# Kernel tuning notes

Hardware: AMD Instinct MI355X
Metric: run time of the kernel (lower is better)

## Reference

```python
import jax, jax.numpy as jnp
import numpy as np

D_MODEL = 1024
HEADS = 16
D_K = D_MODEL // HEADS
D_FF = 4096
EPS = 1e-6


def setup_inputs() -> dict:
    key = jax.random.key(0)
    ks = jax.random.split(key, 20)
    B, S, D = 8, 1024, D_MODEL
    sc = 1.0 / np.sqrt(D)
    scf = 1.0 / np.sqrt(D_FF)
    inp = {
        "x": jax.random.normal(ks[0], (B, S, D), jnp.float32),
        "mask": jnp.ones((B, 1, 1, S), jnp.int32),
        "wq": jax.random.normal(ks[1], (D, D), jnp.float32) * sc,
        "bq": jnp.zeros((D,), jnp.float32),
        "wk": jax.random.normal(ks[2], (D, D), jnp.float32) * sc,
        "bk": jnp.zeros((D,), jnp.float32),
        "wv": jax.random.normal(ks[3], (D, D), jnp.float32) * sc,
        "bv": jnp.zeros((D,), jnp.float32),
        "wo": jax.random.normal(ks[4], (D, D), jnp.float32) * sc,
        "bo": jnp.zeros((D,), jnp.float32),
        "w1": jax.random.normal(ks[5], (D_FF, D), jnp.float32) * sc,
        "b1": jnp.zeros((D_FF,), jnp.float32),
        "w2": jax.random.normal(ks[6], (D, D_FF), jnp.float32) * scf,
        "b2": jnp.zeros((D,), jnp.float32),
        "g1": jnp.ones((D,), jnp.float32),
        "be1": jnp.zeros((D,), jnp.float32),
        "g2": jnp.ones((D,), jnp.float32),
        "be2": jnp.zeros((D,), jnp.float32),
    }
    return inp


def _layernorm(x, gamma, beta):
    # Faithful to custom LayerNorm: unbiased std (ddof=1), divide by (std+eps)
    mean = jnp.mean(x, axis=-1, keepdims=True)
    std = jnp.std(x, axis=-1, ddof=1, keepdims=True)
    return gamma * (x - mean) / (std + EPS) + beta


def _mha(x, mask, wq, bq, wk, bk, wv, bv, wo, bo):
    B, S, D = x.shape
    q = x @ wq.T + bq
    k = x @ wk.T + bk
    v = x @ wv.T + bv
    # [B,S,D] -> [B,H,S,dk]
    q = q.reshape(B, S, HEADS, D_K).transpose(0, 2, 1, 3)
    k = k.reshape(B, S, HEADS, D_K).transpose(0, 2, 1, 3)
    v = v.reshape(B, S, HEADS, D_K).transpose(0, 2, 1, 3)
    scores = jnp.einsum("bhqd,bhkd->bhqk", q, k) / np.sqrt(D_K).astype(np.float32)
    scores = jnp.where(mask == 0, jnp.float32(-1e9), scores)
    attn = jax.nn.softmax(scores, axis=-1)
    out = jnp.einsum("bhqk,bhkd->bhqd", attn, v)
    out = out.transpose(0, 2, 1, 3).reshape(B, S, D)
    return out @ wo.T + bo


def reference(x, mask, wq, bq, wk, bk, wv, bv, wo, bo, w1, b1, w2, b2, g1, be1, g2, be2):
    # residual 1: x + MHA(LN(x))
    h = _layernorm(x, g1, be1)
    x = x + _mha(h, mask, wq, bq, wk, bk, wv, bv, wo, bo)
    # residual 2: x + FFN(LN(x))
    h = _layernorm(x, g2, be2)
    ff = jax.nn.relu(h @ w1.T + b1) @ w2.T + b2
    return x + ff
```

## Files before the change

kernel.cpp:

```cpp
#include <hip/hip_runtime.h>

typedef __attribute__((ext_vector_type(8))) short short8;
typedef __attribute__((ext_vector_type(4))) short short4_t;
typedef __attribute__((ext_vector_type(4))) float floatx4;

#define NTOK 8192
#define S_ 1024
#define DM 1024

__device__ __forceinline__ unsigned short f2b(float f) {
    union { float f; unsigned u; } v; v.f = f;
    unsigned r = v.u + 0x7FFF + ((v.u >> 16) & 1);
    return (unsigned short)(r >> 16);
}

__device__ __forceinline__ void gl_lds16(const unsigned short* g, unsigned short* l) {
    __builtin_amdgcn_global_load_lds((const __attribute__((address_space(1))) void*)g,
                                     (__attribute__((address_space(3))) void*)l, 16, 0, 0);
}

__global__ void cvt_f32_bf16(const float* __restrict__ src, unsigned short* __restrict__ dst, int n) {
    int i = (blockIdx.x * blockDim.x + threadIdx.x) * 4;
    if (i >= n) return;
    float4 v = *reinterpret_cast<const float4*>(src + i);
    short4_t o;
    o.x = (short)f2b(v.x); o.y = (short)f2b(v.y);
    o.z = (short)f2b(v.z); o.w = (short)f2b(v.w);
    *reinterpret_cast<short4_t*>(dst + i) = o;
}

__global__ void copy_f32(const float* __restrict__ src, float* __restrict__ dst, int n) {
    int i = (blockIdx.x * blockDim.x + threadIdx.x) * 4;
    if (i >= n) return;
    *reinterpret_cast<float4*>(dst + i) = *reinterpret_cast<const float4*>(src + i);
}

__global__ __launch_bounds__(256) void ln_kernel(const float* __restrict__ x,
                                                 const float* __restrict__ g,
                                                 const float* __restrict__ be,
                                                 unsigned short* __restrict__ out) {
    const int row = blockIdx.x;
    const int t = threadIdx.x;
    const float4 xv = *reinterpret_cast<const float4*>(x + (size_t)row * DM + t * 4);
    float s = xv.x + xv.y + xv.z + xv.w;
#pragma unroll
    for (int off = 32; off > 0; off >>= 1) s += __shfl_down(s, off);
    __shared__ float red[8];
    const int wid = t >> 6, lane = t & 63;
    if (lane == 0) red[wid] = s;
    __syncthreads();
    const float mean = (red[0] + red[1] + red[2] + red[3]) * (1.f / 1024.f);
    const float dx = xv.x - mean, dy = xv.y - mean, dz = xv.z - mean, dw = xv.w - mean;
    float ss = dx * dx + dy * dy + dz * dz + dw * dw;
#pragma unroll
    for (int off = 32; off > 0; off >>= 1) ss += __shfl_down(ss, off);
    if (lane == 0) red[4 + wid] = ss;
    __syncthreads();
    const float var = (red[4] + red[5] + red[6] + red[7]) * (1.f / 1023.f);
    const float inv = 1.f / (sqrtf(var) + 1e-6f);
    const float4 gv = *reinterpret_cast<const float4*>(g + t * 4);
    const float4 bv = *reinterpret_cast<const float4*>(be + t * 4);
    short4_t o;
    o.x = (short)f2b(gv.x * dx * inv + bv.x);
    o.y = (short)f2b(gv.y * dy * inv + bv.y);
    o.z = (short)f2b(gv.z * dz * inv + bv.z);
    o.w = (short)f2b(gv.w * dw * inv + bv.w);
    *reinterpret_cast<short4_t*>(out + (size_t)row * DM + t * 4) = o;
}

template <int EPI>
__global__ __launch_bounds__(256, 2) void gemm_bt(const unsigned short* __restrict__ A,
                                                  const unsigned short* __restrict__ Bm,
                                                  const float* __restrict__ bias,
                                                  const float* __restrict__ res,
                                                  void* __restrict__ outp,
                                                  int M, int N, int K, int tilesX) {
    __shared__ __align__(16) unsigned short lds[2][2][8192];
    const int t = threadIdx.x;
    const int lane = t & 63, wid = t >> 6;
    const int wr = wid >> 1, wc = wid & 1;

    const int nwg = gridDim.x;
    const int bid = blockIdx.x;
    const int swz = (bid & 7) * (nwg >> 3) + (bid >> 3);
    const int rowBase = (swz / tilesX) * 128;
    const int colBase = (swz % tilesX) * 128;

    const int NT = K >> 6;
    const int lr = lane & 15;
    const int cl = lane >> 4;

    int srow[4], scol[4];
#pragma unroll
    for (int j = 0; j < 4; ++j) {
        const int L = j * 256 + t;
        const int r = L >> 3;
        srow[j] = r;
        scol[j] = ((L & 7) ^ (r & 7)) * 8;
    }

    floatx4 acc[4][4] = {};

#pragma unroll
    for (int j = 0; j < 4; ++j)
        gl_lds16(A + (size_t)(rowBase + srow[j]) * K + scol[j], &lds[0][0][j * 2048 + wid * 512]);
#pragma unroll
    for (int j = 0; j < 4; ++j)
        gl_lds16(Bm + (size_t)(colBase + srow[j]) * K + scol[j], &lds[0][1][j * 2048 + wid * 512]);

    int cur = 0;
    for (int tt = 0; tt < NT; ++tt) {
        if (tt + 1 < NT) {
            const int kk = (tt + 1) << 6;
#pragma unroll
            for (int j = 0; j < 4; ++j)
                gl_lds16(A + (size_t)(rowBase + srow[j]) * K + kk + scol[j],
                         &lds[cur ^ 1][0][j * 2048 + wid * 512]);
#pragma unroll
            for (int j = 0; j < 4; ++j)
                gl_lds16(Bm + (size_t)(colBase + srow[j]) * K + kk + scol[j],
                         &lds[cur ^ 1][1][j * 2048 + wid * 512]);
            asm volatile("s_waitcnt vmcnt(8)" ::: "memory");
        } else {
            asm volatile("s_waitcnt vmcnt(0)" ::: "memory");
        }
        __builtin_amdgcn_s_barrier();
        __builtin_amdgcn_sched_barrier(0);
        const unsigned short* Ab = &lds[cur][0][0];
        const unsigned short* Bb = &lds[cur][1][0];
#pragma unroll
        for (int ks = 0; ks < 2; ++ks) {
            short8 af[4], bfr[4];
#pragma unroll
            for (int m = 0; m < 4; ++m) {
                const int r = wr * 64 + m * 16 + lr;
                const int cp = (ks * 4 + cl) ^ (r & 7);
                af[m] = *reinterpret_cast<const short8*>(&Ab[r * 64 + cp * 8]);
            }
#pragma unroll
            for (int n = 0; n < 4; ++n) {
                const int r = wc * 64 + n * 16 + lr;
                const int cp = (ks * 4 + cl) ^ (r & 7);
                bfr[n] = *reinterpret_cast<const short8*>(&Bb[r * 64 + cp * 8]);
            }
            __builtin_amdgcn_s_setprio(1);
#pragma unroll
            for (int m = 0; m < 4; ++m)
#pragma unroll
                for (int n = 0; n < 4; ++n)
                    acc[m][n] = __builtin_amdgcn_mfma_f32_16x16x32_bf16(af[m], bfr[n], acc[m][n], 0, 0, 0);
            __builtin_amdgcn_s_setprio(0);
        }
        __builtin_amdgcn_sched_barrier(0);
        __builtin_amdgcn_s_barrier();
        cur ^= 1;
    }

    const int lrow = (lane >> 4) * 4, lcol = lane & 15;
    if (EPI == 4) {
        unsigned short* qh = (unsigned short*)outp;
#pragma unroll
        for (int n = 0; n < 4; ++n) {
            const int c = colBase + wc * 64 + n * 16 + lcol;
            const float bn = bias[c];
            const int sect = c >> 10;
            const int hh = (c >> 6) & 15;
            const int dd = c & 63;
#pragma unroll
            for (int m = 0; m < 4; ++m) {
                const int r0 = rowBase + wr * 64 + m * 16 + lrow;
                const int bb = r0 >> 10, ss = r0 & 1023;
                if (sect == 2) {
                    short4_t pk;
#pragma unroll
                    for (int j = 0; j < 4; ++j) pk[j] = (short)f2b(acc[m][n][j] + bn);
                    *reinterpret_cast<short4_t*>(
                        &qh[16777216 + ((size_t)((bb * 16 + hh) * 64 + dd)) * 1024 + ss]) = pk;
                } else {
                    unsigned short* base = qh + sect * 8388608;
#pragma unroll
                    for (int j = 0; j < 4; ++j)
                        base[((size_t)((bb * 16 + hh) * 1024 + ss + j)) * 64 + dd] =
                            f2b(acc[m][n][j] + bn);
                }
            }
        }
        return;
    }
#pragma unroll
    for (int n = 0; n < 4; ++n) {
        const int c = colBase + wc * 64 + n * 16 + lcol;
        const float bn = bias[c];
#pragma unroll
        for (int m = 0; m < 4; ++m) {
#pragma unroll
            for (int j = 0; j < 4; ++j) {
                const int r = rowBase + wr * 64 + m * 16 + lrow + j;
                float v = acc[m][n][j] + bn;
                if (EPI == 1) v += res[(size_t)r * N + c];
                if (EPI == 3) v = fmaxf(v, 0.f);
                if (EPI == 0 || EPI == 1)
                    ((float*)outp)[(size_t)r * N + c] = v;
                else
                    ((unsigned short*)outp)[(size_t)r * N + c] = f2b(v);
            }
        }
    }
}

__global__ __launch_bounds__(256) void attn_mfma(const unsigned short* __restrict__ Qh,
                                                 const unsigned short* __restrict__ Kh,
                                                 const unsigned short* __restrict__ Vt,
                                                 const int* __restrict__ mask,
                                                 unsigned short* __restrict__ out) {
    __shared__ __align__(16) unsigned short Ks[64][72];
    __shared__ __align__(16) unsigned short Vts[64][72];
    __shared__ __align__(16) unsigned short Pbuf[4][16][72];
    __shared__ float msk[64];
    const int t = threadIdx.x;
    const int w = t >> 6, l = t & 63;
    const int g = l >> 4, q16 = l & 15;
    const int bh = blockIdx.y;
    const int qb = blockIdx.x;
    const int b = bh >> 4, h = bh & 15;

    const size_t qbase = ((size_t)bh * 1024 + qb * 64 + w * 16 + q16) * 64;
    const short8 qf0 = *reinterpret_cast<const short8*>(Qh + qbase + g * 8);
    const short8 qf1 = *reinterpret_cast<const short8*>(Qh + qbase + 32 + g * 8);

    floatx4 oacc[4] = {};
    float m_run = -1e30f, l_run = 0.f;

    for (int kc = 0; kc < 16; ++kc) {
        __syncthreads();
#pragma unroll
        for (int s2 = 0; s2 < 2; ++s2) {
            int slot = t + s2 * 256;
            int rr = slot >> 3, cc = (slot & 7) * 8;
            *reinterpret_cast<short8*>(&Ks[rr][cc]) =
                *reinterpret_cast<const short8*>(Kh + ((size_t)bh * 1024 + kc * 64 + rr) * 64 + cc);
            *reinterpret_cast<short8*>(&Vts[rr][cc]) =
                *reinterpret_cast<const short8*>(Vt + ((size_t)bh * 64 + rr) * 1024 + kc * 64 + cc);
        }
        if (t < 64) msk[t] = (mask[b * S_ + kc * 64 + t] == 0) ? -1e9f : 0.f;
        __syncthreads();

        floatx4 st[4] = {};
#pragma unroll
        for (int t4 = 0; t4 < 4; ++t4) {
            short8 kf0 = *reinterpret_cast<const short8*>(&Ks[t4 * 16 + q16][g * 8]);
            short8 kf1 = *reinterpret_cast<const short8*>(&Ks[t4 * 16 + q16][32 + g * 8]);
            st[t4] = __builtin_amdgcn_mfma_f32_16x16x32_bf16(kf0, qf0, st[t4], 0, 0, 0);
            st[t4] = __builtin_amdgcn_mfma_f32_16x16x32_bf16(kf1, qf1, st[t4], 0, 0, 0);
        }
        float sv[4][4];
        float mc = -1e30f;
#pragma unroll
        for (int t4 = 0; t4 < 4; ++t4)
#pragma unroll
            for (int r = 0; r < 4; ++r) {
                float s = st[t4][r] * 0.125f + msk[t4 * 16 + g * 4 + r];
                sv[t4][r] = s;
                mc = fmaxf(mc, s);
            }
        mc = fmaxf(mc, __shfl_xor(mc, 16));
        mc = fmaxf(mc, __shfl_xor(mc, 32));
        const float m_new = fmaxf(m_run, mc);
        const float sc = __expf(m_run - m_new);
        float ps = 0.f;
#pragma unroll
        for (int t4 = 0; t4 < 4; ++t4) {
            short4_t pk;
#pragma unroll
            for (int r = 0; r < 4; ++r) {
                float p = __expf(sv[t4][r] - m_new);
                ps += p;
                pk[r] = (short)f2b(p);
            }
            *reinterpret_cast<short4_t*>(&Pbuf[w][q16][t4 * 16 + g * 4]) = pk;
        }
        ps += __shfl_xor(ps, 16);
        ps += __shfl_xor(ps, 32);
        l_run = l_run * sc + ps;
        m_run = m_new;
#pragma unroll
        for (int r = 0; r < 4; ++r) {
            const float scr = __shfl(sc, g * 4 + r);
#pragma unroll
            for (int n = 0; n < 4; ++n) oacc[n][r] *= scr;
        }
        const short8 pf0 = *reinterpret_cast<const short8*>(&Pbuf[w][q16][g * 8]);
        const short8 pf1 = *reinterpret_cast<const short8*>(&Pbuf[w][q16][32 + g * 8]);
#pragma unroll
        for (int n = 0; n < 4; ++n) {
            short8 vf0 = *reinterpret_cast<const short8*>(&Vts[n * 16 + q16][g * 8]);
            short8 vf1 = *reinterpret_cast<const short8*>(&Vts[n * 16 + q16][32 + g * 8]);
            oacc[n] = __builtin_amdgcn_mfma_f32_16x16x32_bf16(pf0, vf0, oacc[n], 0, 0, 0);
            oacc[n] = __builtin_amdgcn_mfma_f32_16x16x32_bf16(pf1, vf1, oacc[n], 0, 0, 0);
        }
    }
    const float invl = 1.f / l_run;
    const size_t obase = ((size_t)b * S_ + qb * 64 + w * 16) * 1024 + h * 64;
#pragma unroll
    for (int r = 0; r < 4; ++r) {
        const float invr = __shfl(invl, g * 4 + r);
        const size_t orow = obase + (size_t)(g * 4 + r) * 1024;
#pragma unroll
        for (int n = 0; n < 4; ++n)
            out[orow + n * 16 + q16] = f2b(oacc[n][r] * invr);
    }
}

extern "C" void kernel_launch(void* const* d_in, const int* in_sizes, int n_in,
                              void* d_out, int out_size, void* d_ws, size_t ws_size,
                              hipStream_t stream) {
    const float* x   = (const float*)d_in[0];
    const int*  mask = (const int*)d_in[1];
    const float* wq  = (const float*)d_in[2];
    const float* bq  = (const float*)d_in[3];
    const float* wk  = (const float*)d_in[4];
    const float* bk  = (const float*)d_in[5];
    const float* wv  = (const float*)d_in[6];
    const float* bv  = (const float*)d_in[7];
    const float* wo  = (const float*)d_in[8];
    const float* bo  = (const float*)d_in[9];
    const float* w1  = (const float*)d_in[10];
    const float* b1  = (const float*)d_in[11];
    const float* w2  = (const float*)d_in[12];
    const float* b2  = (const float*)d_in[13];
    const float* g1  = (const float*)d_in[14];
    const float* be1 = (const float*)d_in[15];
    const float* g2  = (const float*)d_in[16];
    const float* be2 = (const float*)d_in[17];

    char* ws = (char*)d_ws;
    unsigned short* wqkv_bf = (unsigned short*)(ws);
    unsigned short* wo_bf   = (unsigned short*)(ws + 6291456);
    unsigned short* w1_bf   = (unsigned short*)(ws + 8388608);
    unsigned short* w2_bf   = (unsigned short*)(ws + 16777216);
    float*          bqkv    = (float*)(ws + 25165824);
    unsigned short* h_bf    = (unsigned short*)(ws + 25178112);
    float*          x1      = (float*)(ws + 41955328);
    unsigned short* attn_bf = (unsigned short*)(ws + 75509760);
    unsigned short* qkvh    = (unsigned short*)(ws + 92286976);
    unsigned short* ff1_bf  = (unsigned short*)(ws + 92286976);

    cvt_f32_bf16<<<1024, 256, 0, stream>>>(wq, wqkv_bf, 1048576);
    cvt_f32_bf16<<<1024, 256, 0, stream>>>(wk, wqkv_bf + 1048576, 1048576);
    cvt_f32_bf16<<<1024, 256, 0, stream>>>(wv, wqkv_bf + 2097152, 1048576);
    cvt_f32_bf16<<<1024, 256, 0, stream>>>(wo, wo_bf, 1048576);
    cvt_f32_bf16<<<4096, 256, 0, stream>>>(w1, w1_bf, 4194304);
    cvt_f32_bf16<<<4096, 256, 0, stream>>>(w2, w2_bf, 4194304);
    copy_f32<<<1, 256, 0, stream>>>(bq, bqkv, 1024);
    copy_f32<<<1, 256, 0, stream>>>(bk, bqkv + 1024, 1024);
    copy_f32<<<1, 256, 0, stream>>>(bv, bqkv + 2048, 1024);

    ln_kernel<<<NTOK, 256, 0, stream>>>(x, g1, be1, h_bf);
    gemm_bt<4><<<24 * 64, 256, 0, stream>>>(h_bf, wqkv_bf, bqkv, nullptr, qkvh, NTOK, 3072, 1024, 24);
    attn_mfma<<<dim3(16, 128), 256, 0, stream>>>(qkvh, qkvh + 8388608, qkvh + 16777216, mask, attn_bf);
    gemm_bt<1><<<8 * 64, 256, 0, stream>>>(attn_bf, wo_bf, bo, x, x1, NTOK, 1024, 1024, 8);
    ln_kernel<<<NTOK, 256, 0, stream>>>(x1, g2, be2, h_bf);
    gemm_bt<3><<<32 * 64, 256, 0, stream>>>(h_bf, w1_bf, b1, nullptr, ff1_bf, NTOK, 4096, 1024, 32);
    gemm_bt<1><<<8 * 64, 256, 0, stream>>>(ff1_bf, w2_bf, b2, x1, (float*)d_out, NTOK, 1024, 4096, 8);
}
```

Baseline: 386.2 us.

## Load attention K/V fragments directly from global, skip LDS staging and syncs

The attention kernel now reads K and V MFMA fragments straight from global memory into registers instead of staging them through shared memory with two block barriers per chunk. The mask is precomputed once into a float bias array, and the block index is swizzled so blocks sharing a (batch, head) land on different XCDs. It also adds a lazy-rescale softmax that only updates the running max and rescales the accumulators when the new max exceeds the old one by more than a threshold. The cost is redundant global/L2 traffic, since each wave reloads the same K/V instead of sharing via LDS, plus some numerical risk from the deferred max.

```diff
diff --git a/kernel.cpp b/kernel.cpp
--- a/kernel.cpp
+++ b/kernel.cpp
@@ -33,6 +33,11 @@
     int i = (blockIdx.x * blockDim.x + threadIdx.x) * 4;
     if (i >= n) return;
     *reinterpret_cast<float4*>(dst + i) = *reinterpret_cast<const float4*>(src + i);
+}
+
+__global__ void mask_to_bias(const int* __restrict__ mask, float* __restrict__ mb, int n) {
+    int i = blockIdx.x * blockDim.x + threadIdx.x;
+    if (i < n) mb[i] = (mask[i] == 0) ? -1e9f : 0.f;
 }
 
 __global__ __launch_bounds__(256) void ln_kernel(const float* __restrict__ x,
@@ -211,69 +216,82 @@
 __global__ __launch_bounds__(256) void attn_mfma(const unsigned short* __restrict__ Qh,
                                                  const unsigned short* __restrict__ Kh,
                                                  const unsigned short* __restrict__ Vt,
-                                                 const int* __restrict__ mask,
+                                                 const float* __restrict__ mbias,
                                                  unsigned short* __restrict__ out) {
-    __shared__ __align__(16) unsigned short Ks[64][72];
-    __shared__ __align__(16) unsigned short Vts[64][72];
     __shared__ __align__(16) unsigned short Pbuf[4][16][72];
-    __shared__ float msk[64];
     const int t = threadIdx.x;
     const int w = t >> 6, l = t & 63;
     const int g = l >> 4, q16 = l & 15;
-    const int bh = blockIdx.y;
-    const int qb = blockIdx.x;
+    const int bid = blockIdx.x;
+    const int swz = (bid & 7) * 256 + (bid >> 3);
+    const int bh = swz >> 4, qb = swz & 15;
     const int b = bh >> 4, h = bh & 15;
 
     const size_t qbase = ((size_t)bh * 1024 + qb * 64 + w * 16 + q16) * 64;
     const short8 qf0 = *reinterpret_cast<const short8*>(Qh + qbase + g * 8);
     const short8 qf1 = *reinterpret_cast<const short8*>(Qh + qbase + 32 + g * 8);
 
+    const unsigned short* kp = Kh + (size_t)bh * 65536 + q16 * 64 + g * 8;
+    const unsigned short* vp = Vt + (size_t)bh * 65536 + q16 * 1024 + g * 8;
+    const float* mp = mbias + b * 1024 + g * 4;
+
     floatx4 oacc[4] = {};
     float m_run = -1e30f, l_run = 0.f;
 
     for (int kc = 0; kc < 16; ++kc) {
-        __syncthreads();
-#pragma unroll
-        for (int s2 = 0; s2 < 2; ++s2) {
-            int slot = t + s2 * 256;
-            int rr = slot >> 3, cc = (slot & 7) * 8;
-            *reinterpret_cast<short8*>(&Ks[rr][cc]) =
-                *reinterpret_cast<const short8*>(Kh + ((size_t)bh * 1024 + kc * 64 + rr) * 64 + cc);
-            *reinterpret_cast<short8*>(&Vts[rr][cc]) =
-                *reinterpret_cast<const short8*>(Vt + ((size_t)bh * 64 + rr) * 1024 + kc * 64 + cc);
-        }
-        if (t < 64) msk[t] = (mask[b * S_ + kc * 64 + t] == 0) ? -1e9f : 0.f;
-        __syncthreads();
+        short8 kf0[4], kf1[4];
+#pragma unroll
+        for (int t4 = 0; t4 < 4; ++t4) {
+            kf0[t4] = *reinterpret_cast<const short8*>(kp + kc * 4096 + t4 * 1024);
+            kf1[t4] = *reinterpret_cast<const short8*>(kp + kc * 4096 + t4 * 1024 + 32);
+        }
+        float4 mbv[4];
+#pragma unroll
+        for (int t4 = 0; t4 < 4; ++t4)
+            mbv[t4] = *reinterpret_cast<const float4*>(mp + kc * 64 + t4 * 16);
+        short8 vf0[4], vf1[4];
+#pragma unroll
+        for (int n = 0; n < 4; ++n) {
+            vf0[n] = *reinterpret_cast<const short8*>(vp + n * 16384 + kc * 64);
+            vf1[n] = *reinterpret_cast<const short8*>(vp + n * 16384 + kc * 64 + 32);
+        }
 
         floatx4 st[4] = {};
 #pragma unroll
         for (int t4 = 0; t4 < 4; ++t4) {
-            short8 kf0 = *reinterpret_cast<const short8*>(&Ks[t4 * 16 + q16][g * 8]);
-            short8 kf1 = *reinterpret_cast<const short8*>(&Ks[t4 * 16 + q16][32 + g * 8]);
-            st[t4] = __builtin_amdgcn_mfma_f32_16x16x32_bf16(kf0, qf0, st[t4], 0, 0, 0);
-            st[t4] = __builtin_amdgcn_mfma_f32_16x16x32_bf16(kf1, qf1, st[t4], 0, 0, 0);
-        }
-        float sv[4][4];
+            st[t4] = __builtin_amdgcn_mfma_f32_16x16x32_bf16(kf0[t4], qf0, st[t4], 0, 0, 0);
+            st[t4] = __builtin_amdgcn_mfma_f32_16x16x32_bf16(kf1[t4], qf1, st[t4], 0, 0, 0);
+        }
         float mc = -1e30f;
 #pragma unroll
         for (int t4 = 0; t4 < 4; ++t4)
 #pragma unroll
             for (int r = 0; r < 4; ++r) {
-                float s = st[t4][r] * 0.125f + msk[t4 * 16 + g * 4 + r];
-                sv[t4][r] = s;
+                const float s = st[t4][r] * 0.125f + ((const float*)&mbv[t4])[r];
+                st[t4][r] = s;
                 mc = fmaxf(mc, s);
             }
         mc = fmaxf(mc, __shfl_xor(mc, 16));
         mc = fmaxf(mc, __shfl_xor(mc, 32));
-        const float m_new = fmaxf(m_run, mc);
-        const float sc = __expf(m_run - m_new);
+        if (__any(mc > m_run + 8.f)) {
+            const float m_new = fmaxf(m_run, mc);
+            const float sc = __expf(m_run - m_new);
+            l_run *= sc;
+            m_run = m_new;
+#pragma unroll
+            for (int r = 0; r < 4; ++r) {
+                const float scr = __shfl(sc, g * 4 + r);
+#pragma unroll
+                for (int n = 0; n < 4; ++n) oacc[n][r] *= scr;
+            }
+        }
         float ps = 0.f;
 #pragma unroll
         for (int t4 = 0; t4 < 4; ++t4) {
             short4_t pk;
 #pragma unroll
             for (int r = 0; r < 4; ++r) {
-                float p = __expf(sv[t4][r] - m_new);
+                const float p = __expf(st[t4][r] - m_run);
                 ps += p;
                 pk[r] = (short)f2b(p);
             }
@@ -281,22 +299,14 @@
         }
         ps += __shfl_xor(ps, 16);
         ps += __shfl_xor(ps, 32);
-        l_run = l_run * sc + ps;
-        m_run = m_new;
-#pragma unroll
-        for (int r = 0; r < 4; ++r) {
-            const float scr = __shfl(sc, g * 4 + r);
-#pragma unroll
-            for (int n = 0; n < 4; ++n) oacc[n][r] *= scr;
-        }
+        l_run += ps;
+
         const short8 pf0 = *reinterpret_cast<const short8*>(&Pbuf[w][q16][g * 8]);
         const short8 pf1 = *reinterpret_cast<const short8*>(&Pbuf[w][q16][32 + g * 8]);
 #pragma unroll
         for (int n = 0; n < 4; ++n) {
-            short8 vf0 = *reinterpret_cast<const short8*>(&Vts[n * 16 + q16][g * 8]);
-            short8 vf1 = *reinterpret_cast<const short8*>(&Vts[n * 16 + q16][32 + g * 8]);
-            oacc[n] = __builtin_amdgcn_mfma_f32_16x16x32_bf16(pf0, vf0, oacc[n], 0, 0, 0);
-            oacc[n] = __builtin_amdgcn_mfma_f32_16x16x32_bf16(pf1, vf1, oacc[n], 0, 0, 0);
+            oacc[n] = __builtin_amdgcn_mfma_f32_16x16x32_bf16(pf0, vf0[n], oacc[n], 0, 0, 0);
+            oacc[n] = __builtin_amdgcn_mfma_f32_16x16x32_bf16(pf1, vf1[n], oacc[n], 0, 0, 0);
         }
     }
     const float invl = 1.f / l_run;
@@ -339,11 +349,12 @@
     unsigned short* w1_bf   = (unsigned short*)(ws + 8388608);
     unsigned short* w2_bf   = (unsigned short*)(ws + 16777216);
     float*          bqkv    = (float*)(ws + 25165824);
-    unsigned short* h_bf    = (unsigned short*)(ws + 25178112);
-    float*          x1      = (float*)(ws + 41955328);
-    unsigned short* attn_bf = (unsigned short*)(ws + 75509760);
-    unsigned short* qkvh    = (unsigned short*)(ws + 92286976);
-    unsigned short* ff1_bf  = (unsigned short*)(ws + 92286976);
+    float*          mbias   = (float*)(ws + 25178112);
+    unsigned short* h_bf    = (unsigned short*)(ws + 25210880);
+    float*          x1      = (float*)(ws + 41988096);
+    unsigned short* attn_bf = (unsigned short*)(ws + 75542528);
+    unsigned short* qkvh    = (unsigned short*)(ws + 92319744);
+    unsigned short* ff1_bf  = (unsigned short*)(ws + 92319744);
 
     cvt_f32_bf16<<<1024, 256, 0, stream>>>(wq, wqkv_bf, 1048576);
     cvt_f32_bf16<<<1024, 256, 0, stream>>>(wk, wqkv_bf + 1048576, 1048576);
@@ -354,10 +365,11 @@
     copy_f32<<<1, 256, 0, stream>>>(bq, bqkv, 1024);
     copy_f32<<<1, 256, 0, stream>>>(bk, bqkv + 1024, 1024);
     copy_f32<<<1, 256, 0, stream>>>(bv, bqkv + 2048, 1024);
+    mask_to_bias<<<32, 256, 0, stream>>>(mask, mbias, 8192);
 
     ln_kernel<<<NTOK, 256, 0, stream>>>(x, g1, be1, h_bf);
     gemm_bt<4><<<24 * 64, 256, 0, stream>>>(h_bf, wqkv_bf, bqkv, nullptr, qkvh, NTOK, 3072, 1024, 24);
-    attn_mfma<<<dim3(16, 128), 256, 0, stream>>>(qkvh, qkvh + 8388608, qkvh + 16777216, mask, attn_bf);
+    attn_mfma<<<2048, 256, 0, stream>>>(qkvh, qkvh + 8388608, qkvh + 16777216, mbias, attn_bf);
     gemm_bt<1><<<8 * 64, 256, 0, stream>>>(attn_bf, wo_bf, bo, x, x1, NTOK, 1024, 1024, 8);
     ln_kernel<<<NTOK, 256, 0, stream>>>(x1, g2, be2, h_bf);
     gemm_bt<3><<<32 * 64, 256, 0, stream>>>(h_bf, w1_bf, b1, nullptr, ff1_bf, NTOK, 4096, 1024, 32);
```

New measurement: 537.5 us. 1.39x slower.
